# Performance work log

Measured on AMD Instinct MI355X. Metric: run time of the kernel, lower is better.

The kernel has to match this reference:

```python
import jax, jax.numpy as jnp
import numpy as np

B, N, F_IN, F_OUT, T, K = 32, 512, 64, 64, 12, 3


def setup_inputs() -> dict:
    key = jax.random.key(0)
    k1, k2, k3, k4 = jax.random.split(key, 4)
    x = jax.random.normal(k1, (B, N, F_IN, T), dtype=jnp.float32)
    cheb_polys = jax.random.normal(k2, (K, N, N), dtype=jnp.float32)
    spatial_attention = jax.random.uniform(k3, (B, N, N), dtype=jnp.float32)
    Theta = jax.random.normal(k4, (K, F_IN, F_OUT), dtype=jnp.float32) * 0.1
    return {"x": x, "cheb_polys": cheb_polys, "spatial_attention": spatial_attention, "Theta": Theta}


def reference(x, cheb_polys, spatial_attention, Theta):
    # Original: out[b,n,o,t] = relu( sum_k ( (cheb[k]*att[b]).T @ x[b,:,:,t] ) @ Theta[k] )
    # i.e. out[b,n,o,t] = relu( sum_{k,m,f} cheb[k,m,n]*att[b,m,n]*x[b,m,f,t]*Theta[k,f,o] )
    # Fully vectorized over K and T; einsum picks an efficient contraction path
    # (att-premultiply then batched GEMMs), fusing the nested python loops.
    out = jnp.einsum(
        'kmn,bmn,bmft,kfo->bnot',
        cheb_polys, spatial_attention, x, Theta,
        optimize=True,
    )
    return jax.nn.relu(out)
```

## Files before the change

### kernel.cpp

```cpp
#include <hip/hip_runtime.h>

typedef __attribute__((ext_vector_type(4))) float f32x4;
typedef __attribute__((ext_vector_type(8))) short bf16x8;

typedef __attribute__((address_space(3))) unsigned char lds_b;
typedef const __attribute__((address_space(1))) unsigned char glb_b;

__device__ __forceinline__ void gload_lds16(const void* g, void* l) {
  __builtin_amdgcn_global_load_lds((glb_b*)g, (lds_b*)l, 16, 0, 0);
}

__device__ __forceinline__ unsigned short f2bf(float f) {
  union { float f; unsigned int u; } v; v.f = f;
  unsigned int r = v.u + 0x7fffu + ((v.u >> 16) & 1u);
  return (unsigned short)(r >> 16);
}

__global__ __launch_bounds__(256) void theta_prep_k(const float* __restrict__ Theta,
                                                    unsigned short* __restrict__ Tg) {
  const int tid = threadIdx.x;
#pragma unroll
  for (int j = 0; j < 12; ++j) {
    int i = tid + j * 256;
    int k = i >> 10, rr = i & 1023;
    int f = rr >> 4, o0 = (rr & 15) << 2;
    float4 v = *(const float4*)(Theta + ((size_t)(k * 64 + f)) * 64 + o0);
    float vv[4] = {v.x, v.y, v.z, v.w};
#pragma unroll
    for (int jj = 0; jj < 4; ++jj) {
      int o = o0 + jj;
      int byte = k * 8192 + o * 128 + ((((f >> 3) ^ (o & 7)) << 4) | ((f & 7) << 1));
      *(unsigned short*)((char*)Tg + byte) = f2bf(vv[jj]);
    }
  }
}

__global__ __launch_bounds__(256) void prep_fused_k(const float* __restrict__ x,
                                                    const float* __restrict__ cheb,
                                                    const float* __restrict__ att,
                                                    const unsigned short* __restrict__ Tg,
                                                    unsigned short* __restrict__ A_ws,
                                                    unsigned short* __restrict__ U_ws) {
  __shared__ __align__(16) char smem[24576];
  const int bid = blockIdx.x;
  const int tid = threadIdx.x;

  if (bid < 1024) {
    unsigned short* Xl = (unsigned short*)smem;
    const int xcd = bid & 7, tt = bid >> 3;
    const int l = (tt & ~3) * 8 + xcd * 4 + (tt & 3);
    const int b = l >> 5, mt = l & 31;
    const int m0 = mt * 16;
    const int lane = tid & 63, w = tid >> 6;
    const int c = lane & 15, q = lane >> 4;

    bf16x8 afr[3][2];
#pragma unroll
    for (int k = 0; k < 3; ++k)
#pragma unroll
      for (int h = 0; h < 2; ++h) {
        int g = h * 4 + q;
        afr[k][h] = *(const bf16x8*)((const char*)Tg +
                      k * 8192 + (w * 16 + c) * 128 + (((g ^ (c & 7)) << 4)));
      }

    const float* xb = x + ((size_t)(b * 512 + m0)) * 768;
#pragma unroll
    for (int j = 0; j < 12; ++j) {
      int i = tid + j * 256;
      int m = i / 192, r = i - m * 192;
      float4 v = *(const float4*)(xb + (size_t)m * 768 + r * 4);
      float vv[4] = {v.x, v.y, v.z, v.w};
#pragma unroll
      for (int jj = 0; jj < 4; ++jj) {
        int e = r * 4 + jj;
        int f = e / 12, t = e - f * 12;
        int byte = t * 2048 + m * 128 + ((((f >> 3) ^ (m & 7)) << 4) | ((f & 7) << 1));
        *(unsigned short*)((char*)Xl + byte) = f2bf(vv[jj]);
      }
    }
    __syncthreads();

    const size_t ub0 = ((size_t)(b * 3)) * 768 * 512 + m0 + c;
    for (int t = 0; t < 12; ++t) {
      bf16x8 bfr[2];
#pragma unroll
      for (int h = 0; h < 2; ++h) {
        int g = h * 4 + q;
        bfr[h] = *(const bf16x8*)((char*)Xl + t * 2048 + c * 128 + (((g ^ (c & 7)) << 4)));
      }
#pragma unroll
      for (int k = 0; k < 3; ++k) {
        f32x4 acc = {0.f, 0.f, 0.f, 0.f};
        acc = __builtin_amdgcn_mfma_f32_16x16x32_bf16(afr[k][0], bfr[0], acc, 0, 0, 0);
        acc = __builtin_amdgcn_mfma_f32_16x16x32_bf16(afr[k][1], bfr[1], acc, 0, 0, 0);
        size_t base = ub0 + (size_t)k * 768 * 512 + (size_t)t * 512;
#pragma unroll
        for (int r = 0; r < 4; ++r) {
          int o = w * 16 + q * 4 + r;
          U_ws[base + (size_t)o * 12 * 512] = f2bf(acc[r]);
        }
      }
    }
  } else {
    float (*tile)[68] = (float(*)[68])smem;
    const int id = bid - 1024;
    const int m0 = (id & 7) * 64, n0 = ((id >> 3) & 7) * 64, b = id >> 6;
    const int rm = tid >> 2;
    const int c4 = tid & 3;
    for (int k = 0; k < 3; ++k) {
      const float* cp = cheb + ((size_t)(k * 512 + m0 + rm)) * 512 + n0 + c4 * 16;
      const float* ap = att  + ((size_t)(b * 512 + m0 + rm)) * 512 + n0 + c4 * 16;
#pragma unroll
      for (int j = 0; j < 4; ++j) {
        float4 cc = *(const float4*)(cp + j * 4);
        float4 aa = *(const float4*)(ap + j * 4);
        float4 p; p.x = cc.x * aa.x; p.y = cc.y * aa.y; p.z = cc.z * aa.z; p.w = cc.w * aa.w;
        *(float4*)&tile[rm][c4 * 16 + j * 4] = p;
      }
      __syncthreads();
      unsigned int pk[8];
#pragma unroll
      for (int i = 0; i < 8; ++i) {
        float v0 = tile[c4 * 16 + 2 * i][rm];
        float v1 = tile[c4 * 16 + 2 * i + 1][rm];
        pk[i] = (unsigned int)f2bf(v0) | ((unsigned int)f2bf(v1) << 16);
      }
      unsigned short* op = A_ws + ((size_t)(b * 512 + n0 + rm)) * 1536 + k * 512 + m0 + c4 * 16;
      uint4 w0; w0.x = pk[0]; w0.y = pk[1]; w0.z = pk[2]; w0.w = pk[3];
      uint4 w1; w1.x = pk[4]; w1.y = pk[5]; w1.z = pk[6]; w1.w = pk[7];
      ((uint4*)op)[0] = w0;
      ((uint4*)op)[1] = w1;
      __syncthreads();
    }
  }
}

__global__ __launch_bounds__(256) void gemm_k(const unsigned short* __restrict__ A_ws,
                                              const unsigned short* __restrict__ U_ws,
                                              float* __restrict__ out) {
  __shared__ unsigned short At[128 * 64];
  __shared__ unsigned short Bt[128 * 64];
  const int hw = blockIdx.x;
  const int logical = (hw & 7) * 96 + (hw >> 3);
  const int b = logical / 24;
  const int rem = logical - b * 24;
  const int nb = (rem / 6) * 128;
  const int otb = (rem % 6) * 128;

  const int tid = threadIdx.x;
  const int lane = tid & 63, w = tid >> 6;
  const int wr = w >> 1, wc = w & 1;
  const int q = lane >> 4;
  const int c = lane & 15;

  const int rl = lane >> 3;
  const int gsrc = (lane & 7) ^ rl;
  f32x4 acc[4][4] = {};

  const unsigned short* aRow = A_ws + ((size_t)(b * 512 + nb + w * 8 + rl)) * 1536 + gsrc * 8;
  const int ldsRowBase = w * 8 * 64;

  for (int kt = 0; kt < 24; ++kt) {
    const int k = kt >> 3;
    const int m0k = (kt & 7) << 6;
    const unsigned short* uRow =
        U_ws + ((size_t)((b * 3 + k) * 768 + otb + w * 8 + rl)) * 512 + m0k + gsrc * 8;
#pragma unroll
    for (int i = 0; i < 4; ++i) {
      gload_lds16(aRow + (size_t)(i * 32) * 1536 + kt * 64, &At[ldsRowBase + i * 32 * 64]);
      gload_lds16(uRow + (size_t)(i * 32) * 512,            &Bt[ldsRowBase + i * 32 * 64]);
    }
    __syncthreads();
#pragma unroll
    for (int h = 0; h < 2; ++h) {
      bf16x8 af[4], bfv[4];
#pragma unroll
      for (int mi = 0; mi < 4; ++mi) {
        int row = wr * 64 + mi * 16 + c;
        af[mi] = *(const bf16x8*)&At[row * 64 + (((h * 4 + q) ^ (row & 7)) << 3)];
      }
#pragma unroll
      for (int ni = 0; ni < 4; ++ni) {
        int row = wc * 64 + ni * 16 + c;
        bfv[ni] = *(const bf16x8*)&Bt[row * 64 + (((h * 4 + q) ^ (row & 7)) << 3)];
      }
#pragma unroll
      for (int mi = 0; mi < 4; ++mi)
#pragma unroll
        for (int ni = 0; ni < 4; ++ni)
          acc[mi][ni] = __builtin_amdgcn_mfma_f32_16x16x32_bf16(af[mi], bfv[ni], acc[mi][ni], 0, 0, 0);
    }
    __syncthreads();
  }
#pragma unroll
  for (int mi = 0; mi < 4; ++mi) {
#pragma unroll
    for (int r = 0; r < 4; ++r) {
      int n = nb + wr * 64 + mi * 16 + q * 4 + r;
      float* orow = out + ((size_t)(b * 512 + n)) * 768 + otb + wc * 64 + c;
#pragma unroll
      for (int ni = 0; ni < 4; ++ni)
        orow[ni * 16] = fmaxf(acc[mi][ni][r], 0.f);
    }
  }
}

__global__ __launch_bounds__(256) void fallback_k(const float* __restrict__ x,
                                                  const float* __restrict__ cheb,
                                                  const float* __restrict__ att,
                                                  const float* __restrict__ Theta,
                                                  float* __restrict__ out) {
  __shared__ float wsm[3][512];
  __shared__ float z[3][768];
  const int n = blockIdx.x, b = blockIdx.y;
  const int tid = threadIdx.x;
  for (int i = tid; i < 1536; i += 256) {
    int k = i >> 9, m = i & 511;
    wsm[k][m] = cheb[((size_t)(k * 512 + m)) * 512 + n] * att[((size_t)(b * 512 + m)) * 512 + n];
  }
  __syncthreads();
  float a0[3] = {0.f, 0.f, 0.f}, a1[3] = {0.f, 0.f, 0.f}, a2[3] = {0.f, 0.f, 0.f};
  const float* xb = x + (size_t)b * 512 * 768;
  for (int m = 0; m < 512; ++m) {
    float w0 = wsm[0][m], w1 = wsm[1][m], w2 = wsm[2][m];
    float x0 = xb[(size_t)m * 768 + tid];
    float x1 = xb[(size_t)m * 768 + tid + 256];
    float x2 = xb[(size_t)m * 768 + tid + 512];
    a0[0] += w0 * x0; a0[1] += w1 * x0; a0[2] += w2 * x0;
    a1[0] += w0 * x1; a1[1] += w1 * x1; a1[2] += w2 * x1;
    a2[0] += w0 * x2; a2[1] += w1 * x2; a2[2] += w2 * x2;
  }
#pragma unroll
  for (int k = 0; k < 3; ++k) {
    z[k][tid] = a0[k]; z[k][tid + 256] = a1[k]; z[k][tid + 512] = a2[k];
  }
  __syncthreads();
#pragma unroll
  for (int j = 0; j < 3; ++j) {
    int ot = tid + j * 256;
    int o = ot / 12, t = ot - o * 12;
    float s = 0.f;
    for (int k = 0; k < 3; ++k)
#pragma unroll
      for (int f = 0; f < 64; ++f)
        s += z[k][f * 12 + t] * Theta[((size_t)(k * 64 + f)) * 64 + o];
    out[((size_t)(b * 512 + n)) * 768 + ot] = fmaxf(s, 0.f);
  }
}

extern "C" void kernel_launch(void* const* d_in, const int* in_sizes, int n_in,
                              void* d_out, int out_size, void* d_ws, size_t ws_size,
                              hipStream_t stream) {
  const float* x     = (const float*)d_in[0];
  const float* cheb  = (const float*)d_in[1];
  const float* att   = (const float*)d_in[2];
  const float* Theta = (const float*)d_in[3];
  float* out = (float*)d_out;

  const size_t needA = (size_t)32 * 512 * 1536 * 2;
  const size_t needU = (size_t)32 * 3 * 768 * 512 * 2;
  const size_t needT = (size_t)3 * 64 * 64 * 2;

  if (ws_size >= needA + needU + needT) {
    unsigned short* A_ws = (unsigned short*)d_ws;
    unsigned short* U_ws = (unsigned short*)((char*)d_ws + needA);
    unsigned short* Tg   = (unsigned short*)((char*)d_ws + needA + needU);
    theta_prep_k<<<dim3(1), 256, 0, stream>>>(Theta, Tg);
    prep_fused_k<<<dim3(3072), 256, 0, stream>>>(x, cheb, att, Tg, A_ws, U_ws);
    gemm_k<<<dim3(768), 256, 0, stream>>>(A_ws, U_ws, out);
  } else {
    fallback_k<<<dim3(512, 32), 256, 0, stream>>>(x, cheb, att, Theta, out);
  }
}
```

Measured before the change: 111.9 us.

## Store U workspace in m-tile-blocked layout for contiguous MFMA output writes

The U intermediate is now laid out blocked by (b,k,m-tile,t) with 16-wide m chunks contiguous per output feature. The prep kernel writes each 16x16 MFMA result as contiguous runs instead of scattered 2-byte stores strided by 12*512 elements, and the main GEMM's gather addresses are recomputed to match. The XCD-aware block remapping in the prep kernel is dropped. The cost is more complex per-row offset computation and 16-byte global-to-LDS loads that now come from scattered 16-element chunks.

```diff
diff --git a/kernel.cpp b/kernel.cpp
--- a/kernel.cpp
+++ b/kernel.cpp
@@ -47,9 +47,7 @@
 
   if (bid < 1024) {
     unsigned short* Xl = (unsigned short*)smem;
-    const int xcd = bid & 7, tt = bid >> 3;
-    const int l = (tt & ~3) * 8 + xcd * 4 + (tt & 3);
-    const int b = l >> 5, mt = l & 31;
+    const int b = bid >> 5, mt = bid & 31;
     const int m0 = mt * 16;
     const int lane = tid & 63, w = tid >> 6;
     const int c = lane & 15, q = lane >> 4;
@@ -81,7 +79,7 @@
     }
     __syncthreads();
 
-    const size_t ub0 = ((size_t)(b * 3)) * 768 * 512 + m0 + c;
+    const int ub0 = w * 256 + q * 64 + c;
     for (int t = 0; t < 12; ++t) {
       bf16x8 bfr[2];
 #pragma unroll
@@ -94,12 +92,11 @@
         f32x4 acc = {0.f, 0.f, 0.f, 0.f};
         acc = __builtin_amdgcn_mfma_f32_16x16x32_bf16(afr[k][0], bfr[0], acc, 0, 0, 0);
         acc = __builtin_amdgcn_mfma_f32_16x16x32_bf16(afr[k][1], bfr[1], acc, 0, 0, 0);
-        size_t base = ub0 + (size_t)k * 768 * 512 + (size_t)t * 512;
-#pragma unroll
-        for (int r = 0; r < 4; ++r) {
-          int o = w * 16 + q * 4 + r;
-          U_ws[base + (size_t)o * 12 * 512] = f2bf(acc[r]);
-        }
+        unsigned short* up = U_ws +
+            ((size_t)(((b * 3 + k) * 32 + mt) * 12 + t)) * 1024 + ub0;
+#pragma unroll
+        for (int r = 0; r < 4; ++r)
+          up[r * 16] = f2bf(acc[r]);
       }
     }
   } else {
@@ -156,20 +153,30 @@
 
   const int rl = lane >> 3;
   const int gsrc = (lane & 7) ^ rl;
+  const int mi0 = (gsrc & 1) * 8;
+  const int mtq = gsrc >> 1;
   f32x4 acc[4][4] = {};
+
+  int ot_off[4];
+#pragma unroll
+  for (int i = 0; i < 4; ++i) {
+    int rr = otb + w * 8 + rl + i * 32;
+    int o = rr / 12, t = rr - 12 * o;
+    ot_off[i] = t * 1024 + o * 16 + mi0;
+  }
 
   const unsigned short* aRow = A_ws + ((size_t)(b * 512 + nb + w * 8 + rl)) * 1536 + gsrc * 8;
   const int ldsRowBase = w * 8 * 64;
 
   for (int kt = 0; kt < 24; ++kt) {
     const int k = kt >> 3;
-    const int m0k = (kt & 7) << 6;
-    const unsigned short* uRow =
-        U_ws + ((size_t)((b * 3 + k) * 768 + otb + w * 8 + rl)) * 512 + m0k + gsrc * 8;
+    const int mc = kt & 7;
+    const unsigned short* uBase =
+        U_ws + ((size_t)((b * 3 + k) * 32 + mc * 4 + mtq)) * 12288;
 #pragma unroll
     for (int i = 0; i < 4; ++i) {
       gload_lds16(aRow + (size_t)(i * 32) * 1536 + kt * 64, &At[ldsRowBase + i * 32 * 64]);
-      gload_lds16(uRow + (size_t)(i * 32) * 512,            &Bt[ldsRowBase + i * 32 * 64]);
+      gload_lds16(uBase + ot_off[i],                        &Bt[ldsRowBase + i * 32 * 64]);
     }
     __syncthreads();
 #pragma unroll
```

Measured after the change: 120.5 us. 7.7% more time.
